# Performance work log

Hardware: AMD Instinct MI355X
Metric: run time of the kernel (lower is better)

Reference implementation:

```python
import jax, jax.numpy as jnp
import numpy as np

EPS = 1e-8

def setup_inputs() -> dict:
    key = jax.random.key(0)
    k1, k2, k3, k4 = jax.random.split(key, 4)
    b, in_c, out_c, style_c, k, h, w = 8, 512, 512, 512, 3, 64, 64
    return {
        "input": jax.random.normal(k1, (b, in_c, h, w), dtype=jnp.float32),
        "style": jax.random.normal(k2, (b, style_c), dtype=jnp.float32),
        "w_affine": jax.random.normal(k3, (in_c, style_c), dtype=jnp.float32),  # Linear weight, init N(0,1), runtime-scaled
        "b_affine": jnp.ones((1, in_c), dtype=jnp.float32),                     # Bias init_value=1.0
        "w_conv": jax.random.normal(k4, (out_c, in_c, k, k), dtype=jnp.float32),
    }

def reference(input, style, w_affine, b_affine, w_conv):
    b, in_c, h, w = input.shape
    out_c, _, kh, kw = w_conv.shape
    # Equalized-LR runtime scales (lr_mul=1):
    affine_scale = 1.0 / (w_affine.shape[1] ** 0.5)          # he_std for Linear
    conv_scale = 1.0 / ((in_c * kh * kw) ** 0.5)             # he_std for conv weight
    # affine: Linear + Bias (bias initialized to 1.0)
    s = style @ w_affine.T * affine_scale + b_affine          # [b, in_c]
    # modulate: per-sample weight tensor [b, out_c, in_c, kh, kw]
    wgt = s[:, None, :, None, None] * (w_conv * conv_scale)[None]
    # demodulate
    demod = jax.lax.rsqrt(jnp.sum(wgt * wgt, axis=(2, 3, 4), keepdims=True) + EPS)
    wgt = wgt * demod
    # grouped conv with groups = batch (stride=1, padding=1)
    x = input.reshape(1, b * in_c, h, w)
    wgt = wgt.reshape(b * out_c, in_c, kh, kw)
    out = jax.lax.conv_general_dilated(
        x, wgt,
        window_strides=(1, 1),
        padding=[(1, 1), (1, 1)],
        dimension_numbers=("NCHW", "OIHW", "NCHW"),
        feature_group_count=b,
    )
    return out.reshape(b, out_c, h, w)
```

## Files before the change

### kernel.cpp

```cpp
#include <hip/hip_runtime.h>
#include <hip/hip_bf16.h>

#define BB 8
#define CIN 512
#define COUT 512
#define HH 64
#define WW 64

#define AFF_SCALE 0.044194173824159216f
#define CONV_SCALE 0.014731391274719736f
#define CONV_SCALE2 (1.0f/4608.0f)

typedef short s16x8 __attribute__((ext_vector_type(8)));
typedef float f32x16 __attribute__((ext_vector_type(16)));

__device__ __forceinline__ unsigned short f2bf(float f) {
  __hip_bfloat16 h = __float2bfloat16(f);
  return *reinterpret_cast<unsigned short*>(&h);
}

__device__ __forceinline__ void gload_lds16(const void* g, void* l) {
  __builtin_amdgcn_global_load_lds(
      (const __attribute__((address_space(1))) unsigned int*)g,
      (__attribute__((address_space(3))) unsigned int*)l, 16, 0, 0);
}

__global__ __launch_bounds__(256) void affine_kernel(
    const float* __restrict__ style, const float* __restrict__ wa,
    const float* __restrict__ ba, float* __restrict__ smod) {
  int wid  = (blockIdx.x << 2) + (threadIdx.x >> 6);
  int lane = threadIdx.x & 63;
  int b  = wid >> 9;
  int ic = wid & 511;
  const float* s = style + b * CIN;
  const float* w = wa + (size_t)ic * CIN;
  float sum = 0.f;
#pragma unroll
  for (int k = 0; k < CIN / 64; ++k) sum += s[lane + 64 * k] * w[lane + 64 * k];
#pragma unroll
  for (int off = 32; off; off >>= 1) sum += __shfl_down(sum, off, 64);
  if (lane == 0) smod[wid] = sum * AFF_SCALE + ba[ic];
}

__global__ __launch_bounds__(256) void wsq_kernel(
    const float* __restrict__ wc, float* __restrict__ wsq) {
  int i = blockIdx.x * 256 + threadIdx.x;
  const float* p = wc + (size_t)i * 9;
  float s = 0.f;
#pragma unroll
  for (int k = 0; k < 9; ++k) { float v = p[k]; s += v * v; }
  wsq[i] = s;
}

__global__ __launch_bounds__(256) void demod_kernel(
    const float* __restrict__ smod, const float* __restrict__ wsq,
    float* __restrict__ demod) {
  int wid  = (blockIdx.x << 2) + (threadIdx.x >> 6);
  int lane = threadIdx.x & 63;
  int b  = wid >> 9;
  int oc = wid & 511;
  const float* s = smod + b * CIN;
  const float* w = wsq + (size_t)oc * CIN;
  float sum = 0.f;
#pragma unroll
  for (int k = 0; k < CIN / 64; ++k) {
    float sv = s[lane + 64 * k];
    sum += sv * sv * w[lane + 64 * k];
  }
#pragma unroll
  for (int off = 32; off; off >>= 1) sum += __shfl_down(sum, off, 64);
  if (lane == 0) demod[wid] = rsqrtf(sum * CONV_SCALE2 + 1e-8f) * CONV_SCALE;
}

__global__ __launch_bounds__(256) void premod_kernel(
    const float* __restrict__ xin, const float* __restrict__ smod,
    ushort* __restrict__ xt) {
  int n = blockIdx.x * 256 + threadIdx.x;
  int kg = n & 3;
  int x  = (n >> 2) & 63;
  int y  = (n >> 8) & 63;
  int g  = (n >> 14) & 15;
  int b  = n >> 18;
  int ic0 = g * 32 + kg * 8;
  const float* sp = smod + b * CIN + ic0;
  const float* xp = xin + (((size_t)b * CIN + ic0) * HH + y) * WW + x;
  s16x8 o;
#pragma unroll
  for (int j = 0; j < 8; ++j) {
    float v = xp[(size_t)j * HH * WW] * sp[j];
    o[j] = (short)f2bf(v);
  }
  *(s16x8*)(xt + (size_t)n * 8) = o;
}

__global__ __launch_bounds__(256) void wpack_kernel(
    const float* __restrict__ wc, ushort* __restrict__ wfrag) {
  int n = blockIdx.x * 256 + threadIdx.x;
  int l    = n & 63;
  int ks   = (n >> 6) & 1;
  int mf   = (n >> 7) & 15;
  int widx = n >> 11;
  int g = widx / 9, tap = widx % 9;
  int kh = tap / 3, kw = tap - kh * 3;
  int oc  = mf * 32 + (l & 31);
  int ic0 = g * 32 + ks * 16 + 8 * (l >> 5);
  s16x8 o;
#pragma unroll
  for (int j = 0; j < 8; ++j) {
    float v = wc[((size_t)oc * CIN + ic0 + j) * 9 + kh * 3 + kw];
    o[j] = (short)f2bf(v);
  }
  *(s16x8*)(wfrag + (size_t)n * 8) = o;
}

#define XS_ROW 4224
#define XS_BUF (6 * XS_ROW)

__global__ __launch_bounds__(256, 2) void conv_mfma(
    const ushort* __restrict__ xt,
    const ushort* __restrict__ wfrag,
    const float* __restrict__ demod,
    float* __restrict__ out) {
  __shared__ char lds[2 * XS_BUF];

  int tid = threadIdx.x;
  int l = tid & 63, w = tid >> 6;
  int wm = w >> 1, wr = w & 1;
  int bid = blockIdx.x;
  int ocb = bid & 3;
  int b   = (bid >> 2) & 7;
  int yt  = bid >> 5;
  int y0  = yt * 4;

  f32x16 acc[2][4];
#pragma unroll
  for (int i = 0; i < 2; ++i)
#pragma unroll
    for (int j = 0; j < 4; ++j)
#pragma unroll
      for (int e = 0; e < 16; ++e) acc[i][j][e] = 0.f;

  if (tid < 96) {
    int buf = tid & 1, side = (tid >> 1) & 1, kgz = (tid >> 2) & 3, r = tid >> 4;
    int chunk = side ? (260 + kgz) : kgz;
    *(int4*)(lds + buf * XS_BUF + r * XS_ROW + chunk * 16) = int4{0, 0, 0, 0};
  }
  if (y0 == 0) {
    for (int i = tid; i < 512; i += 256) {
      int buf = i & 1, chunk = 4 + (i >> 1);
      *(int4*)(lds + buf * XS_BUF + chunk * 16) = int4{0, 0, 0, 0};
    }
  }
  if (y0 == 60) {
    for (int i = tid; i < 512; i += 256) {
      int buf = i & 1, chunk = 4 + (i >> 1);
      *(int4*)(lds + buf * XS_BUF + 5 * XS_ROW + chunk * 16) = int4{0, 0, 0, 0};
    }
  }

  int boffs[2][3][2];
  {
    int lm = l & 31, kh2 = l >> 5;
#pragma unroll
    for (int ph = 0; ph < 2; ++ph)
#pragma unroll
      for (int dxi = 0; dxi < 3; ++dxi)
#pragma unroll
        for (int ks = 0; ks < 2; ++ks) {
          int col = ph * 32 + lm + dxi;
          int kg  = kh2 + 2 * ks;
          boffs[ph][dxi][ks] = (col * 4 + (kg ^ ((col >> 1) & 3))) * 16;
        }
  }

  int col_s = 1 + w * 16 + (l >> 2);
  int srcoff = (col_s - 1) * 64 + ((l & 3) ^ ((col_s >> 1) & 3)) * 16;
  int lds_woff = 64 + w * 1024;

  const char* xtb = (const char*)xt;
  const char* wl = (const char*)wfrag + (size_t)(ocb * 4 + wm * 2) * 2048 + (size_t)l * 16;

  s16x8 wH[3][2];
#pragma unroll
  for (int q = 0; q < 2; ++q) wH[0][q] = *(const s16x8*)(wl + q * 2048);
#pragma unroll
  for (int q = 0; q < 2; ++q) wH[1][q] = *(const s16x8*)(wl + q * 2048 + 1024);

  {
    size_t gbase = (size_t)(b * 16) * 262144;
#pragma unroll
    for (int r = 0; r < 6; ++r) {
      int gy = y0 - 1 + r;
      if (gy >= 0 && gy < HH)
        gload_lds16(xtb + gbase + (size_t)gy * 4096 + srcoff,
                    lds + r * XS_ROW + lds_woff);
    }
  }
  __syncthreads();

  s16x8 bfr0[2][4];
  s16x8 bfr1[4];

  for (int g2 = 0; g2 < 8; ++g2) {
    const char* wg = wl + (size_t)g2 * 589824;
#pragma unroll
    for (int gg = 0; gg < 2; ++gg) {
      char* xs_r = lds + gg * XS_BUF;
      char* xs_w = lds + (gg ^ 1) * XS_BUF;
#pragma unroll
      for (int tap = 0; tap < 9; ++tap) {
        const int X0 = 2 * (gg * 9 + tap);
        const int dy = tap / 3 - 1, dxi = tap % 3;
        const int rb = wr * 2 + 1 + dy;

        if (tap == 0) {
#pragma unroll
          for (int dr = 0; dr < 2; ++dr)
#pragma unroll
            for (int ph = 0; ph < 2; ++ph)
              bfr0[0][dr * 2 + ph] =
                  *(const s16x8*)(xs_r + (rb + dr) * XS_ROW + boffs[ph][dxi][0]);
        }

        if (tap == 6 && (gg == 0 || g2 < 7)) {
          __builtin_amdgcn_sched_barrier(0);
          size_t gbase = (size_t)(b * 16 + g2 * 2 + gg + 1) * 262144;
#pragma unroll
          for (int r = 0; r < 6; ++r) {
            int gy = y0 - 1 + r;
            if (gy >= 0 && gy < HH)
              gload_lds16(xtb + gbase + (size_t)gy * 4096 + srcoff,
                          xs_w + r * XS_ROW + lds_woff);
          }
          __builtin_amdgcn_sched_barrier(0);
        }

#pragma unroll
        for (int dr = 0; dr < 2; ++dr)
#pragma unroll
          for (int ph = 0; ph < 2; ++ph)
            bfr1[dr * 2 + ph] =
                *(const s16x8*)(xs_r + (rb + dr) * XS_ROW + boffs[ph][dxi][1]);

        {
          const char* wp = wg + (size_t)((X0 + 2) >> 1) * 32768 + ((X0 + 2) & 1) * 1024;
#pragma unroll
          for (int q = 0; q < 2; ++q)
            wH[(X0 + 2) % 3][q] = *(const s16x8*)(wp + q * 2048);
          __builtin_amdgcn_s_setprio(1);
#pragma unroll
          for (int q = 0; q < 2; ++q)
#pragma unroll
            for (int n = 0; n < 4; ++n)
              acc[q][n] = __builtin_amdgcn_mfma_f32_32x32x16_bf16(
                  wH[X0 % 3][q], bfr0[tap & 1][n], acc[q][n], 0, 0, 0);
          __builtin_amdgcn_s_setprio(0);
        }

        if (tap < 8) {
          const int dyn = (tap + 1) / 3 - 1, dxn = (tap + 1) % 3;
          const int rbn = wr * 2 + 1 + dyn;
#pragma unroll
          for (int dr = 0; dr < 2; ++dr)
#pragma unroll
            for (int ph = 0; ph < 2; ++ph)
              bfr0[(tap + 1) & 1][dr * 2 + ph] =
                  *(const s16x8*)(xs_r + (rbn + dr) * XS_ROW + boffs[ph][dxn][0]);
        }

        {
          const char* wp = wg + (size_t)((X0 + 3) >> 1) * 32768 + ((X0 + 3) & 1) * 1024;
#pragma unroll
          for (int q = 0; q < 2; ++q)
            wH[(X0 + 3) % 3][q] = *(const s16x8*)(wp + q * 2048);
          __builtin_amdgcn_s_setprio(1);
#pragma unroll
          for (int q = 0; q < 2; ++q)
#pragma unroll
            for (int n = 0; n < 4; ++n)
              acc[q][n] = __builtin_amdgcn_mfma_f32_32x32x16_bf16(
                  wH[(X0 + 1) % 3][q], bfr1[n], acc[q][n], 0, 0, 0);
          __builtin_amdgcn_s_setprio(0);
        }

        if (tap == 8 && (gg == 0 || g2 < 7)) {
          __builtin_amdgcn_sched_barrier(0);
          asm volatile("s_waitcnt vmcnt(4)" ::: "memory");
          __builtin_amdgcn_sched_barrier(0);
          __builtin_amdgcn_s_barrier();
          __builtin_amdgcn_sched_barrier(0);
        }
      }
    }
  }

  int gy_base = y0 + wr * 2;
  int colbase = l & 31;
  int rowadd = 4 * (l >> 5);
#pragma unroll
  for (int q = 0; q < 2; ++q) {
#pragma unroll
    for (int reg = 0; reg < 16; ++reg) {
      int row = (reg & 3) + 8 * (reg >> 2) + rowadd;
      int oc = ocb * 128 + (wm * 2 + q) * 32 + row;
      float dm = demod[b * COUT + oc];
#pragma unroll
      for (int n = 0; n < 4; ++n) {
        int gy = gy_base + (n >> 1);
        int px = (n & 1) * 32 + colbase;
        out[((size_t)(b * COUT + oc)) * 4096 + gy * 64 + px] = acc[q][n][reg] * dm;
      }
    }
  }
}

extern "C" void kernel_launch(void* const* d_in, const int* in_sizes, int n_in,
                              void* d_out, int out_size, void* d_ws, size_t ws_size,
                              hipStream_t stream) {
  const float* input = (const float*)d_in[0];
  const float* style = (const float*)d_in[1];
  const float* wa    = (const float*)d_in[2];
  const float* ba    = (const float*)d_in[3];
  const float* wconv = (const float*)d_in[4];
  float* out = (float*)d_out;

  float* smod  = (float*)d_ws;
  float* demod = smod + BB * CIN;
  float* wsq   = demod + BB * COUT;
  ushort* wfrag = (ushort*)(wsq + (size_t)COUT * CIN);
  ushort* xt    = wfrag + (size_t)16 * 9 * 32 * 64 * 8;

  affine_kernel<<<BB * CIN / 4, 256, 0, stream>>>(style, wa, ba, smod);
  wsq_kernel<<<COUT * CIN / 256, 256, 0, stream>>>(wconv, wsq);
  demod_kernel<<<BB * COUT / 4, 256, 0, stream>>>(smod, wsq, demod);
  wpack_kernel<<<16 * 9 * 32 * 64 / 256, 256, 0, stream>>>(wconv, wfrag);
  premod_kernel<<<BB * 16 * 64 * 64 * 4 / 256, 256, 0, stream>>>(input, smod, xt);
  conv_mfma<<<BB * 4 * 16, 256, 0, stream>>>(xt, wfrag, demod, out);
}
```

Baseline: 156.2 us.

## Reorder conv taps by row to reuse LDS B fragments across vertical taps

The inner 9-tap loop is rewritten as a hand-scheduled macro sequence that walks taps column-wise (dy varies fastest) with three rotating B-fragment slots. Input rows loaded from LDS are shared between adjacent dy taps, which cuts LDS reads per group. Weight prefetch grows to four register sets that stay two half-steps ahead, and the vmcnt wait is relaxed to match. The trade is more VGPRs and a fragile explicit schedule, which could hurt occupancy at the two-blocks-per-CU launch bound.

```diff
diff --git a/kernel.cpp b/kernel.cpp
--- a/kernel.cpp
+++ b/kernel.cpp
@@ -116,6 +116,78 @@
 #define XS_ROW 4224
 #define XS_BUF (6 * XS_ROW)
 
+#define MFMA1(A_, B_, C_) __builtin_amdgcn_mfma_f32_32x32x16_bf16(A_, B_, C_, 0, 0, 0)
+
+#define MH(W_, SX, SY, kf) \
+  __builtin_amdgcn_s_setprio(1); \
+  acc[0][0] = MFMA1(W_[0], SX[0 + (kf)], acc[0][0]); \
+  acc[1][0] = MFMA1(W_[1], SX[0 + (kf)], acc[1][0]); \
+  acc[0][1] = MFMA1(W_[0], SX[2 + (kf)], acc[0][1]); \
+  acc[1][1] = MFMA1(W_[1], SX[2 + (kf)], acc[1][1]); \
+  acc[0][2] = MFMA1(W_[0], SY[0 + (kf)], acc[0][2]); \
+  acc[1][2] = MFMA1(W_[1], SY[0 + (kf)], acc[1][2]); \
+  acc[0][3] = MFMA1(W_[0], SY[2 + (kf)], acc[0][3]); \
+  acc[1][3] = MFMA1(W_[1], SY[2 + (kf)], acc[1][3]); \
+  __builtin_amdgcn_s_setprio(0);
+
+#define WPRE(W_, POFF, KS) \
+  W_[0] = *(const s16x8*)(wg + (size_t)(POFF) * 32768 + (KS) * 1024); \
+  W_[1] = *(const s16x8*)(wg + (size_t)(POFF) * 32768 + 2048 + (KS) * 1024);
+
+#define LOADSLOT(S, RR, DXI) \
+  S[0] = *(const s16x8*)(xs_r + (wr2 + (RR)) * XS_ROW + addrV[0][DXI][0]); \
+  S[1] = *(const s16x8*)(xs_r + (wr2 + (RR)) * XS_ROW + addrV[0][DXI][1]); \
+  S[2] = *(const s16x8*)(xs_r + (wr2 + (RR)) * XS_ROW + addrV[1][DXI][0]); \
+  S[3] = *(const s16x8*)(xs_r + (wr2 + (RR)) * XS_ROW + addrV[1][DXI][1]);
+
+#define GBARRIER \
+  __builtin_amdgcn_sched_barrier(0); \
+  asm volatile("s_waitcnt vmcnt(16)" ::: "memory"); \
+  __builtin_amdgcn_sched_barrier(0); \
+  __builtin_amdgcn_s_barrier(); \
+  __builtin_amdgcn_sched_barrier(0);
+
+#define GBODY(GG, E0, E1, O0, O1, TAILC) \
+{ \
+  const char* xs_r = (const char*)lds + (GG) * XS_BUF; \
+  char* xs_w = lds + ((GG) ^ 1) * XS_BUF; \
+  const char* wg = wl + (size_t)(g2 * 18 + (GG) * 9) * 32768; \
+  LOADSLOT(bA, 0, 0) LOADSLOT(bB, 1, 0) \
+   MH(E0, bA, bB, 0) WPRE(E0, 6, 0) LOADSLOT(bC, 2, 0) \
+         MH(E1, bA, bB, 1) WPRE(E1, 6, 1) \
+   MH(O0, bB, bC, 0) WPRE(O0, 1, 0) LOADSLOT(bA, 3, 0) \
+         MH(O1, bB, bC, 1) WPRE(O1, 1, 1) \
+   MH(E0, bC, bA, 0) WPRE(E0, 4, 0) LOADSLOT(bB, 0, 1) \
+         MH(E1, bC, bA, 1) WPRE(E1, 4, 1) LOADSLOT(bC, 1, 1) \
+   MH(O0, bB, bC, 0) WPRE(O0, 7, 0) LOADSLOT(bA, 2, 1) \
+         MH(O1, bB, bC, 1) WPRE(O1, 7, 1) \
+   MH(E0, bC, bA, 0) WPRE(E0, 2, 0) LOADSLOT(bB, 3, 1) \
+         MH(E1, bC, bA, 1) WPRE(E1, 2, 1) \
+   if (TAILC) stage6(xtb, (size_t)(b * 16 + g2 * 2 + (GG) + 1) * 262144, srcoff, xs_w, lds_woff, y0); \
+         MH(O0, bA, bB, 0) WPRE(O0, 5, 0) LOADSLOT(bC, 0, 2) \
+         MH(O1, bA, bB, 1) WPRE(O1, 5, 1) LOADSLOT(bA, 1, 2) \
+   MH(E0, bC, bA, 0) WPRE(E0, 8, 0) LOADSLOT(bB, 2, 2) \
+         MH(E1, bC, bA, 1) WPRE(E1, 8, 1) \
+   MH(O0, bA, bB, 0) WPRE(O0, 9, 0) LOADSLOT(bC, 3, 2) \
+         MH(O1, bA, bB, 1) WPRE(O1, 9, 1) \
+   MH(E0, bB, bC, 0) WPRE(E0, 12, 0) \
+         MH(E1, bB, bC, 1) WPRE(E1, 12, 1) \
+  if (TAILC) { GBARRIER } \
+}
+
+__device__ __forceinline__ void stage6(const char* xtb, size_t gbase, int srcoff,
+                                       char* xs_w, int lds_woff, int y0) {
+  __builtin_amdgcn_sched_barrier(0);
+#pragma unroll
+  for (int r = 0; r < 6; ++r) {
+    int gy = y0 - 1 + r;
+    if (gy >= 0 && gy < HH)
+      gload_lds16(xtb + gbase + (size_t)gy * 4096 + srcoff,
+                  xs_w + r * XS_ROW + lds_woff);
+  }
+  __builtin_amdgcn_sched_barrier(0);
+}
+
 __global__ __launch_bounds__(256, 2) void conv_mfma(
     const ushort* __restrict__ xt,
     const ushort* __restrict__ wfrag,
@@ -126,6 +198,7 @@
   int tid = threadIdx.x;
   int l = tid & 63, w = tid >> 6;
   int wm = w >> 1, wr = w & 1;
+  int wr2 = wr * 2;
   int bid = blockIdx.x;
   int ocb = bid & 3;
   int b   = (bid >> 2) & 7;
@@ -158,7 +231,7 @@
     }
   }
 
-  int boffs[2][3][2];
+  int addrV[2][3][2];
   {
     int lm = l & 31, kh2 = l >> 5;
 #pragma unroll
@@ -169,7 +242,7 @@
         for (int ks = 0; ks < 2; ++ks) {
           int col = ph * 32 + lm + dxi;
           int kg  = kh2 + 2 * ks;
-          boffs[ph][dxi][ks] = (col * 4 + (kg ^ ((col >> 1) & 3))) * 16;
+          addrV[ph][dxi][ks] = (col * 4 + (kg ^ ((col >> 1) & 3))) * 16;
         }
   }
 
@@ -180,11 +253,11 @@
   const char* xtb = (const char*)xt;
   const char* wl = (const char*)wfrag + (size_t)(ocb * 4 + wm * 2) * 2048 + (size_t)l * 16;
 
-  s16x8 wH[3][2];
-#pragma unroll
-  for (int q = 0; q < 2; ++q) wH[0][q] = *(const s16x8*)(wl + q * 2048);
-#pragma unroll
-  for (int q = 0; q < 2; ++q) wH[1][q] = *(const s16x8*)(wl + q * 2048 + 1024);
+  s16x8 wHa[2], wHb[2], wHc[2], wHd[2];
+  wHa[0] = *(const s16x8*)(wl);                       wHa[1] = *(const s16x8*)(wl + 2048);
+  wHb[0] = *(const s16x8*)(wl + 1024);                wHb[1] = *(const s16x8*)(wl + 3072);
+  wHc[0] = *(const s16x8*)(wl + 3 * 32768);           wHc[1] = *(const s16x8*)(wl + 3 * 32768 + 2048);
+  wHd[0] = *(const s16x8*)(wl + 3 * 32768 + 1024);    wHd[1] = *(const s16x8*)(wl + 3 * 32768 + 3072);
 
   {
     size_t gbase = (size_t)(b * 16) * 262144;
@@ -198,103 +271,14 @@
   }
   __syncthreads();
 
-  s16x8 bfr0[2][4];
-  s16x8 bfr1[4];
+  s16x8 bA[4], bB[4], bC[4];
 
   for (int g2 = 0; g2 < 8; ++g2) {
-    const char* wg = wl + (size_t)g2 * 589824;
-#pragma unroll
-    for (int gg = 0; gg < 2; ++gg) {
-      char* xs_r = lds + gg * XS_BUF;
-      char* xs_w = lds + (gg ^ 1) * XS_BUF;
-#pragma unroll
-      for (int tap = 0; tap < 9; ++tap) {
-        const int X0 = 2 * (gg * 9 + tap);
-        const int dy = tap / 3 - 1, dxi = tap % 3;
-        const int rb = wr * 2 + 1 + dy;
-
-        if (tap == 0) {
-#pragma unroll
-          for (int dr = 0; dr < 2; ++dr)
-#pragma unroll
-            for (int ph = 0; ph < 2; ++ph)
-              bfr0[0][dr * 2 + ph] =
-                  *(const s16x8*)(xs_r + (rb + dr) * XS_ROW + boffs[ph][dxi][0]);
-        }
-
-        if (tap == 6 && (gg == 0 || g2 < 7)) {
-          __builtin_amdgcn_sched_barrier(0);
-          size_t gbase = (size_t)(b * 16 + g2 * 2 + gg + 1) * 262144;
-#pragma unroll
-          for (int r = 0; r < 6; ++r) {
-            int gy = y0 - 1 + r;
-            if (gy >= 0 && gy < HH)
-              gload_lds16(xtb + gbase + (size_t)gy * 4096 + srcoff,
-                          xs_w + r * XS_ROW + lds_woff);
-          }
-          __builtin_amdgcn_sched_barrier(0);
-        }
-
-#pragma unroll
-        for (int dr = 0; dr < 2; ++dr)
-#pragma unroll
-          for (int ph = 0; ph < 2; ++ph)
-            bfr1[dr * 2 + ph] =
-                *(const s16x8*)(xs_r + (rb + dr) * XS_ROW + boffs[ph][dxi][1]);
-
-        {
-          const char* wp = wg + (size_t)((X0 + 2) >> 1) * 32768 + ((X0 + 2) & 1) * 1024;
-#pragma unroll
-          for (int q = 0; q < 2; ++q)
-            wH[(X0 + 2) % 3][q] = *(const s16x8*)(wp + q * 2048);
-          __builtin_amdgcn_s_setprio(1);
-#pragma unroll
-          for (int q = 0; q < 2; ++q)
-#pragma unroll
-            for (int n = 0; n < 4; ++n)
-              acc[q][n] = __builtin_amdgcn_mfma_f32_32x32x16_bf16(
-                  wH[X0 % 3][q], bfr0[tap & 1][n], acc[q][n], 0, 0, 0);
-          __builtin_amdgcn_s_setprio(0);
-        }
-
-        if (tap < 8) {
-          const int dyn = (tap + 1) / 3 - 1, dxn = (tap + 1) % 3;
-          const int rbn = wr * 2 + 1 + dyn;
-#pragma unroll
-          for (int dr = 0; dr < 2; ++dr)
-#pragma unroll
-            for (int ph = 0; ph < 2; ++ph)
-              bfr0[(tap + 1) & 1][dr * 2 + ph] =
-                  *(const s16x8*)(xs_r + (rbn + dr) * XS_ROW + boffs[ph][dxn][0]);
-        }
-
-        {
-          const char* wp = wg + (size_t)((X0 + 3) >> 1) * 32768 + ((X0 + 3) & 1) * 1024;
-#pragma unroll
-          for (int q = 0; q < 2; ++q)
-            wH[(X0 + 3) % 3][q] = *(const s16x8*)(wp + q * 2048);
-          __builtin_amdgcn_s_setprio(1);
-#pragma unroll
-          for (int q = 0; q < 2; ++q)
-#pragma unroll
-            for (int n = 0; n < 4; ++n)
-              acc[q][n] = __builtin_amdgcn_mfma_f32_32x32x16_bf16(
-                  wH[(X0 + 1) % 3][q], bfr1[n], acc[q][n], 0, 0, 0);
-          __builtin_amdgcn_s_setprio(0);
-        }
-
-        if (tap == 8 && (gg == 0 || g2 < 7)) {
-          __builtin_amdgcn_sched_barrier(0);
-          asm volatile("s_waitcnt vmcnt(4)" ::: "memory");
-          __builtin_amdgcn_sched_barrier(0);
-          __builtin_amdgcn_s_barrier();
-          __builtin_amdgcn_sched_barrier(0);
-        }
-      }
-    }
-  }
-
-  int gy_base = y0 + wr * 2;
+    GBODY(0, wHa, wHb, wHc, wHd, true)
+    GBODY(1, wHc, wHd, wHa, wHb, (g2 < 7))
+  }
+
+  int gy_base = y0 + wr2;
   int colbase = l & 31;
   int rowadd = 4 * (l >> 5);
 #pragma unroll
```

New measurement: 152.8 us. -2.2%, faster.
